# Kernel optimization log

Hardware: AMD Instinct MI355X
Metric: run time of the kernel (lower is better)

Reference implementation:

```python
import jax, jax.numpy as jnp
import numpy as np
import math

B, N = 1, 768
C_S, C_Z, C_H, H, P_QK, P_V = 256, 128, 128, 8, 8, 12
EPS, INF, LN_EPS = 1e-8, 1e5, 1e-5


def _quat_to_rot(q):
    # q: [..., 4] normalized quaternion (w, x, y, z) -> [..., 3, 3]
    w, x, y, z = jnp.moveaxis(q, -1, 0)
    r = jnp.stack([
        1 - 2 * (y * y + z * z), 2 * (x * y - w * z), 2 * (x * z + w * y),
        2 * (x * y + w * z), 1 - 2 * (x * x + z * z), 2 * (y * z - w * x),
        2 * (x * z - w * y), 2 * (y * z + w * x), 1 - 2 * (x * x + y * y),
    ], axis=-1)
    return r.reshape(q.shape[:-1] + (3, 3))


def _ln(x, g, b):
    mu = x.mean(-1, keepdims=True)
    var = ((x - mu) ** 2).mean(-1, keepdims=True)
    return (x - mu) * jax.lax.rsqrt(var + LN_EPS) * g + b


def setup_inputs():
    key = jax.random.key(0)
    ks = jax.random.split(key, 20)
    inp = {}
    inp['s'] = jax.random.normal(ks[0], (B, N, C_S), jnp.float32)
    inp['p'] = jax.random.normal(ks[1], (B, N, N, C_Z), jnp.float32)
    q = jax.random.normal(ks[2], (B, N, 4), jnp.float32)
    inp['rot'] = _quat_to_rot(q / jnp.linalg.norm(q, axis=-1, keepdims=True))
    inp['trans'] = 10.0 * jax.random.normal(ks[3], (B, N, 3), jnp.float32)
    inp['mask'] = jnp.ones((B, N), jnp.float32)
    concat_dim = H * C_H + H * P_V * 4 + H * C_Z
    dims = {'q': (H * C_H, C_S), 'kv': (2 * H * C_H, C_S), 'qp': (H * P_QK * 3, C_S),
            'kvp': (H * (P_QK + P_V) * 3, C_S), 'pb': (H, C_Z), 'o': (C_S, concat_dim),
            't1': (C_S, C_S), 't2': (C_S, C_S), 't3': (C_S, C_S), 'bb': (6, C_S)}
    i = 4
    for nm, (do, di) in dims.items():
        k1, k2 = jax.random.split(ks[i]); i += 1
        inp['W' + nm] = 0.02 * jax.random.normal(k1, (do, di), jnp.float32)
        inp['b' + nm] = 0.02 * jax.random.normal(k2, (do,), jnp.float32)
    inp['head_w'] = 0.1 * jax.random.normal(ks[i], (H,), jnp.float32)
    inp['g1'] = jnp.ones((C_S,), jnp.float32)
    inp['be1'] = jnp.zeros((C_S,), jnp.float32)
    inp['g2'] = jnp.ones((C_S,), jnp.float32)
    inp['be2'] = jnp.zeros((C_S,), jnp.float32)
    return inp


def reference(s, p, rot, trans, mask, Wq, bq, Wkv, bkv, Wqp, bqp, Wkvp, bkvp,
              Wpb, bpb, Wo, bo, Wt1, bt1, Wt2, bt2, Wt3, bt3, Wbb, bbb,
              head_w, g1, be1, g2, be2):
    # ---------------- Invariant Point Attention ----------------
    q = (s @ Wq.T + bq).reshape(B, N, H, C_H)
    kv = (s @ Wkv.T + bkv).reshape(B, N, H, 2 * C_H)
    k, v = kv[..., :C_H], kv[..., C_H:]
    # points: linear output is coordinate-major (x-block, y-block, z-block)
    qp = (s @ Wqp.T + bqp).reshape(B, N, 3, H, P_QK)
    qp = jnp.einsum('bnij,bnjhp->bnhpi', rot, qp) + trans[:, :, None, None, :]
    kvp = (s @ Wkvp.T + bkvp).reshape(B, N, 3, H, P_QK + P_V)
    kvp = jnp.einsum('bnij,bnjhp->bnhpi', rot, kvp) + trans[:, :, None, None, :]
    kp, vp = kvp[..., :P_QK, :], kvp[..., P_QK:, :]
    bias_p = p @ Wpb.T + bpb  # [B,N,N,H]
    a = jnp.einsum('bihc,bjhc->bhij', q, k) * math.sqrt(1.0 / (3 * C_H))
    a = a + math.sqrt(1.0 / 3) * jnp.transpose(bias_p, (0, 3, 1, 2))
    d2 = ((qp[:, :, None] - kp[:, None]) ** 2).sum(-1)  # [B,N,N,H,Pqk]
    hw = jax.nn.softplus(head_w) * math.sqrt(1.0 / (3 * (P_QK * 9.0 / 2)))
    pt_att = -0.5 * (d2 * hw[None, None, None, :, None]).sum(-1)  # [B,N,N,H]
    m2 = mask[:, :, None] * mask[:, None, :]
    a = a + jnp.transpose(pt_att, (0, 3, 1, 2)) + (INF * (m2 - 1.0))[:, None]
    att = jax.nn.softmax(a, axis=-1)  # [B,H,N,N]
    o = jnp.einsum('bhij,bjhc->bihc', att, v).reshape(B, N, H * C_H)
    opt = jnp.einsum('bhij,bjhpx->bihpx', att, vp)  # [B,N,H,Pv,3] global
    opt = jnp.einsum('bnji,bnhpj->bnhpi', rot, opt - trans[:, :, None, None, :])
    opt_norm = jnp.sqrt((opt ** 2).sum(-1) + EPS).reshape(B, N, H * P_V)
    opt_flat = jnp.moveaxis(opt.reshape(B, N, H * P_V, 3), -1, -2).reshape(B, N, 3 * H * P_V)
    opair = jnp.einsum('bhij,bijz->bihz', att, p).reshape(B, N, H * C_Z)
    ipa_out = jnp.concatenate([o, opt_flat, opt_norm, opair], -1) @ Wo.T + bo
    # residual + dropout(eval: identity) + LayerNorm
    s1 = _ln(s + ipa_out, g1, be1)
    # ---------------- StructureTransition (1 layer) ----------------
    x = jax.nn.relu(s1 @ Wt1.T + bt1)
    x = jax.nn.relu(x @ Wt2.T + bt2)
    s2 = _ln(s1 + (x @ Wt3.T + bt3), g2, be2)
    # ---------------- BackboneUpdate + masked quaternion compose ----------------
    upd = (s2 @ Wbb.T + bbb) * mask[..., None]  # [B,N,6]
    qvec = jnp.concatenate([jnp.ones(upd.shape[:-1] + (1,), upd.dtype), upd[..., :3]], -1)
    qvec = qvec / jnp.linalg.norm(qvec, axis=-1, keepdims=True)
    rot_new = jnp.einsum('bnij,bnjk->bnik', rot, _quat_to_rot(qvec))
    trans_new = trans + jnp.einsum('bnij,bnj->bni', rot, upd[..., 3:])
    return (s2, rot_new, trans_new)
```

## Files before the change

kernel.cpp:

```cpp
#include <hip/hip_runtime.h>
#include <hip/hip_bf16.h>
#include <math.h>

#define NN 768
#define CS 256
#define CZ 128
#define CH 128
#define HH 8
#define PQK 8
#define PV 12
#define CONCAT 2432
#define ATT_HSTRIDE (768*768)

typedef __bf16 v8bf __attribute__((ext_vector_type(8)));
typedef __bf16 v4bf __attribute__((ext_vector_type(4)));
typedef float  v4f  __attribute__((ext_vector_type(4)));

__device__ inline unsigned short f2bf(float f) {
    union { float f; unsigned u; } v; v.f = f;
    unsigned r = v.u + 0x7FFFu + ((v.u >> 16) & 1u);
    return (unsigned short)(r >> 16);
}
__device__ inline float bf2f(unsigned short u) {
    union { unsigned u; float f; } v; v.u = ((unsigned)u) << 16; return v.f;
}
__device__ inline unsigned encf(float f) {
    unsigned u = __float_as_uint(f);
    return (u >> 31) ? ~u : (u | 0x80000000u);
}
__device__ inline float decf(unsigned e) {
    unsigned u = (e >> 31) ? (e & 0x7FFFFFFFu) : ~e;
    return __uint_as_float(u);
}

#define NCVT 9
struct CvtDesc {
    const float* src[NCVT];
    unsigned short* dst[NCVT];
    int nelem[NCVT];
    int blk_start[NCVT + 1];
};

__global__ __launch_bounds__(256) void cvt_many(CvtDesc d)
{
    int b = blockIdx.x;
    int seg = 0;
    #pragma unroll
    for (int i = 0; i < NCVT - 1; i++) if (b >= d.blk_start[i + 1]) seg = i + 1;
    int local = b - d.blk_start[seg];
    int base = local * 2048 + threadIdx.x;
    const float* s = d.src[seg];
    unsigned short* o = d.dst[seg];
    int n = d.nelem[seg];
    #pragma unroll
    for (int r = 0; r < 8; r++) {
        int idx = base + r * 256;
        if (idx < n) o[idx] = f2bf(s[idx]);
    }
}

struct ProjDesc {
    const unsigned short* W[4];
    const float* bias[4];
    unsigned short* dstb[4];
    float* dstf[4];
    int D[4];
    int ldc[4];
    int mode[4];
    int blk_start[5];
};

__global__ __launch_bounds__(256) void proj_all(const unsigned short* __restrict__ A, ProjDesc d)
{
    __shared__ unsigned short As[64][40];
    __shared__ unsigned short Ws[64][40];
    int bx = blockIdx.x;
    int seg = 0;
    #pragma unroll
    for (int q = 0; q < 3; q++) if (bx >= d.blk_start[q + 1]) seg = q + 1;
    int bd = (bx - d.blk_start[seg]) * 64;
    int bi = blockIdx.y * 64;
    const unsigned short* W = d.W[seg];
    int D = d.D[seg], ldc = d.ldc[seg];

    int tid = threadIdx.x, lane = tid & 63, wid = tid >> 6;
    int wr = (wid >> 1) * 32, wc = (wid & 1) * 32;
    v4f acc[2][2] = {};
    int lrow = tid >> 2, lcol = (tid & 3) * 8;
    const unsigned short* Ap = A + (size_t)(bi + lrow) * 256 + lcol;
    const unsigned short* Wp = W + (size_t)(bd + lrow) * 256 + lcol;
    bool wv = (bd + lrow) < D;
    int fr = lane & 15, fc = (lane >> 4) * 8;

    for (int k0 = 0; k0 < 256; k0 += 32) {
        *(int4*)&As[lrow][lcol] = *(const int4*)(Ap + k0);
        int4 wz = {0, 0, 0, 0};
        *(int4*)&Ws[lrow][lcol] = wv ? *(const int4*)(Wp + k0) : wz;
        __syncthreads();
        v8bf a0 = *(const v8bf*)&As[wr + fr][fc];
        v8bf a1 = *(const v8bf*)&As[wr + 16 + fr][fc];
        v8bf b0 = *(const v8bf*)&Ws[wc + fr][fc];
        v8bf b1 = *(const v8bf*)&Ws[wc + 16 + fr][fc];
        acc[0][0] = __builtin_amdgcn_mfma_f32_16x16x32_bf16(a0, b0, acc[0][0], 0, 0, 0);
        acc[0][1] = __builtin_amdgcn_mfma_f32_16x16x32_bf16(a0, b1, acc[0][1], 0, 0, 0);
        acc[1][0] = __builtin_amdgcn_mfma_f32_16x16x32_bf16(a1, b0, acc[1][0], 0, 0, 0);
        acc[1][1] = __builtin_amdgcn_mfma_f32_16x16x32_bf16(a1, b1, acc[1][1], 0, 0, 0);
        __syncthreads();
    }
    const float* bias = d.bias[seg];
    int mode = d.mode[seg];
    unsigned short* Cb = d.dstb[seg];
    float* Cf = d.dstf[seg];
    int mrow = (lane >> 4) * 4;
    #pragma unroll
    for (int mi = 0; mi < 2; mi++) {
        #pragma unroll
        for (int ni = 0; ni < 2; ni++) {
            int dd = bd + wc + ni * 16 + fr;
            if (dd < D) {
                #pragma unroll
                for (int r = 0; r < 4; r++) {
                    int m = bi + wr + mi * 16 + mrow + r;
                    float v = acc[mi][ni][r] + bias[dd];
                    if (mode == 2) Cb[(size_t)m * ldc + dd] = f2bf(v);
                    else           Cf[(size_t)m * ldc + dd] = v;
                }
            }
        }
    }
}

template<int SPLITK, int MODE, int RELU>
__global__ __launch_bounds__(256) void mfma_gemm(
    const unsigned short* __restrict__ A,
    const unsigned short* __restrict__ W,
    const float* __restrict__ bias,
    float* __restrict__ C,
    unsigned short* __restrict__ Cb,
    int D, int K, int ldc)
{
    __shared__ unsigned short As[64][40];
    __shared__ unsigned short Ws[64][40];
    int tid = threadIdx.x;
    int bi = blockIdx.y * 64;
    int bd = blockIdx.x * 64;
    int kpb = K / SPLITK;
    int k0b = blockIdx.z * kpb;
    int lane = tid & 63;
    int wid = tid >> 6;
    int wr = (wid >> 1) * 32, wc = (wid & 1) * 32;
    v4f acc[2][2] = {};
    int lrow = tid >> 2;
    int lcol = (tid & 3) * 8;
    const unsigned short* Ap = A + (size_t)(bi + lrow) * K + lcol;
    const unsigned short* Wp = W + (size_t)(bd + lrow) * K + lcol;
    bool wv = (bd + lrow) < D;
    int fr = lane & 15, fc = (lane >> 4) * 8;

    for (int k0 = k0b; k0 < k0b + kpb; k0 += 32) {
        *(int4*)&As[lrow][lcol] = *(const int4*)(Ap + k0);
        int4 wz = {0, 0, 0, 0};
        *(int4*)&Ws[lrow][lcol] = wv ? *(const int4*)(Wp + k0) : wz;
        __syncthreads();
        v8bf a0 = *(const v8bf*)&As[wr + fr][fc];
        v8bf a1 = *(const v8bf*)&As[wr + 16 + fr][fc];
        v8bf b0 = *(const v8bf*)&Ws[wc + fr][fc];
        v8bf b1 = *(const v8bf*)&Ws[wc + 16 + fr][fc];
        acc[0][0] = __builtin_amdgcn_mfma_f32_16x16x32_bf16(a0, b0, acc[0][0], 0, 0, 0);
        acc[0][1] = __builtin_amdgcn_mfma_f32_16x16x32_bf16(a0, b1, acc[0][1], 0, 0, 0);
        acc[1][0] = __builtin_amdgcn_mfma_f32_16x16x32_bf16(a1, b0, acc[1][0], 0, 0, 0);
        acc[1][1] = __builtin_amdgcn_mfma_f32_16x16x32_bf16(a1, b1, acc[1][1], 0, 0, 0);
        __syncthreads();
    }
    int mrow = (lane >> 4) * 4;
    #pragma unroll
    for (int mi = 0; mi < 2; mi++) {
        #pragma unroll
        for (int ni = 0; ni < 2; ni++) {
            int d = bd + wc + ni * 16 + fr;
            if (d < D) {
                #pragma unroll
                for (int r = 0; r < 4; r++) {
                    int m = bi + wr + mi * 16 + mrow + r;
                    float v = acc[mi][ni][r];
                    if (SPLITK > 1) {
                        atomicAdd(&C[(size_t)m * ldc + d], v);
                    } else {
                        v += bias[d];
                        if (RELU) v = fmaxf(v, 0.f);
                        if (MODE != 2) C[(size_t)m * ldc + d] = v;
                        if (MODE >= 1) Cb[(size_t)m * ldc + d] = f2bf(v);
                    }
                }
            }
        }
    }
}

__global__ __launch_bounds__(256) void prep2_kernel(
    const float* __restrict__ qpraw, const float* __restrict__ kvpraw,
    const float* __restrict__ rot, const float* __restrict__ trans,
    const unsigned short* __restrict__ kv_bf,
    unsigned short* __restrict__ qph, unsigned short* __restrict__ qpl,
    unsigned short* __restrict__ kph, unsigned short* __restrict__ kpl,
    unsigned short* __restrict__ Vc)
{
    __shared__ unsigned short tile[32][136];
    int bx = blockIdx.x;
    int t = threadIdx.x;
    if (bx < 672) {
        int id = bx*256 + t;
        int i = id / (HH*28);
        int rem = id % (HH*28);
        int h = rem / 28;
        int idx = rem % 28;
        const float* R = rot + i*9;
        const float* T = trans + i*3;
        float s0, s1, s2;
        if (idx < 8) {
            s0 = qpraw[i*192 +   0 + h*8 + idx];
            s1 = qpraw[i*192 +  64 + h*8 + idx];
            s2 = qpraw[i*192 + 128 + h*8 + idx];
        } else {
            int pp = idx - 8;
            s0 = kvpraw[i*480 +   0 + h*20 + pp];
            s1 = kvpraw[i*480 + 160 + h*20 + pp];
            s2 = kvpraw[i*480 + 320 + h*20 + pp];
        }
        float ov[3];
        ov[0] = R[0]*s0 + R[1]*s1 + R[2]*s2 + T[0];
        ov[1] = R[3]*s0 + R[4]*s1 + R[5]*s2 + T[1];
        ov[2] = R[6]*s0 + R[7]*s1 + R[8]*s2 + T[2];
        if (idx < 8) {
            #pragma unroll
            for (int x = 0; x < 3; x++) {
                unsigned short hi = f2bf(ov[x]);
                qph[i*256 + h*32 + idx*3 + x] = hi;
                qpl[i*256 + h*32 + idx*3 + x] = f2bf(ov[x] - bf2f(hi));
            }
            if (idx == 0) {
                #pragma unroll
                for (int m = 24; m < 32; m++) { qph[i*256+h*32+m] = 0; qpl[i*256+h*32+m] = 0; }
            }
        } else if (idx < 16) {
            int pp = idx - 8;
            #pragma unroll
            for (int x = 0; x < 3; x++) {
                unsigned short hi = f2bf(ov[x]);
                kph[i*256 + h*32 + pp*3 + x] = hi;
                kpl[i*256 + h*32 + pp*3 + x] = f2bf(ov[x] - bf2f(hi));
            }
            if (idx == 8) {
                #pragma unroll
                for (int m = 24; m < 32; m++) { kph[i*256+h*32+m] = 0; kpl[i*256+h*32+m] = 0; }
            }
        } else {
            int ppv = idx - 16;
            #pragma unroll
            for (int x = 0; x < 3; x++)
                Vc[((size_t)h*192 + 128 + ppv*3 + x)*768 + i] = f2bf(ov[x]);
        }
    } else {
        int bx2 = bx - 672;
        int h = bx2 & 7, jt = bx2 >> 3;
        int r = t >> 3, c0 = (t & 7) * 16;
        const unsigned short* src = kv_bf + (size_t)(jt*32 + r)*2048 + h*256 + 128 + c0;
        *(int4*)&tile[r][c0]     = *(const int4*)src;
        *(int4*)&tile[r][c0 + 8] = *(const int4*)(src + 8);
        __syncthreads();
        int c = t >> 1, jh = (t & 1) * 16;
        unsigned short tmp[16];
        #pragma unroll
        for (int k = 0; k < 16; k++) tmp[k] = tile[jh + k][c];
        unsigned short* dst = Vc + ((size_t)h*192 + c)*768 + jt*32 + jh;
        *(int4*)dst       = *(int4*)&tmp[0];
        *(int4*)(dst + 8) = *(int4*)&tmp[8];
    }
}

__global__ __launch_bounds__(256) void logits_mfma(
    const unsigned short* __restrict__ q_bf, const unsigned short* __restrict__ kv_bf,
    const unsigned short* __restrict__ qph, const unsigned short* __restrict__ qpl,
    const unsigned short* __restrict__ kph, const unsigned short* __restrict__ kpl,
    const float* __restrict__ mask, const float* __restrict__ head_w,
    float* __restrict__ att, unsigned* __restrict__ m0enc)
{
    __shared__ unsigned short Qs[64][136];
    __shared__ unsigned short Ks[64][136];
    __shared__ unsigned short Aph[64][40], Apl[64][40], Bph[64][40], Bpl[64][40];
    __shared__ float Qss[64], Kss[64], Mi[64], Mj[64];
    int h = blockIdx.z;
    int i0 = blockIdx.y * 64, j0 = blockIdx.x * 64;
    int tid = threadIdx.x, lane = tid & 63, wid = tid >> 6;
    int wr = (wid >> 1) * 32, wc = (wid & 1) * 32;
    int r = tid >> 2, cq = (tid & 3) * 32;
    const unsigned short* qg = q_bf  + (size_t)(i0 + r)*1024 + h*128 + cq;
    const unsigned short* kg = kv_bf + (size_t)(j0 + r)*2048 + h*256 + cq;
    #pragma unroll
    for (int kk = 0; kk < 4; kk++) {
        *(int4*)&Qs[r][cq + kk*8] = *(const int4*)(qg + kk*8);
        *(int4*)&Ks[r][cq + kk*8] = *(const int4*)(kg + kk*8);
    }
    int cp = (tid & 3) * 8;
    *(int4*)&Aph[r][cp] = *(const int4*)(qph + (size_t)(i0 + r)*256 + h*32 + cp);
    *(int4*)&Apl[r][cp] = *(const int4*)(qpl + (size_t)(i0 + r)*256 + h*32 + cp);
    *(int4*)&Bph[r][cp] = *(const int4*)(kph + (size_t)(j0 + r)*256 + h*32 + cp);
    *(int4*)&Bpl[r][cp] = *(const int4*)(kpl + (size_t)(j0 + r)*256 + h*32 + cp);
    if (tid < 64) {
        Mi[tid] = mask[i0 + tid];
        Mj[tid] = mask[j0 + tid];
    }
    __syncthreads();
    if (tid < 64) {
        float qs2 = 0.f, ks2 = 0.f;
        #pragma unroll
        for (int m = 0; m < 24; m++) {
            float qv = bf2f(Aph[tid][m]) + bf2f(Apl[tid][m]);
            float kv = bf2f(Bph[tid][m]) + bf2f(Bpl[tid][m]);
            qs2 += qv*qv; ks2 += kv*kv;
        }
        Qss[tid] = qs2; Kss[tid] = ks2;
    }
    int fr = lane & 15, fc = (lane >> 4) * 8;
    v4f aqk[2][2] = {}, ap[2][2] = {};
    #pragma unroll
    for (int ks = 0; ks < 4; ks++) {
        v8bf a0 = *(const v8bf*)&Qs[wr + fr][ks*32 + fc];
        v8bf a1 = *(const v8bf*)&Qs[wr + 16 + fr][ks*32 + fc];
        v8bf b0 = *(const v8bf*)&Ks[wc + fr][ks*32 + fc];
        v8bf b1 = *(const v8bf*)&Ks[wc + 16 + fr][ks*32 + fc];
        aqk[0][0] = __builtin_amdgcn_mfma_f32_16x16x32_bf16(a0, b0, aqk[0][0], 0, 0, 0);
        aqk[0][1] = __builtin_amdgcn_mfma_f32_16x16x32_bf16(a0, b1, aqk[0][1], 0, 0, 0);
        aqk[1][0] = __builtin_amdgcn_mfma_f32_16x16x32_bf16(a1, b0, aqk[1][0], 0, 0, 0);
        aqk[1][1] = __builtin_amdgcn_mfma_f32_16x16x32_bf16(a1, b1, aqk[1][1], 0, 0, 0);
    }
    {
        v8bf ah0 = *(const v8bf*)&Aph[wr + fr][fc];
        v8bf ah1 = *(const v8bf*)&Aph[wr + 16 + fr][fc];
        v8bf al0 = *(const v8bf*)&Apl[wr + fr][fc];
        v8bf al1 = *(const v8bf*)&Apl[wr + 16 + fr][fc];
        v8bf bh0 = *(const v8bf*)&Bph[wc + fr][fc];
        v8bf bh1 = *(const v8bf*)&Bph[wc + 16 + fr][fc];
        v8bf bl0 = *(const v8bf*)&Bpl[wc + fr][fc];
        v8bf bl1 = *(const v8bf*)&Bpl[wc + 16 + fr][fc];
        ap[0][0] = __builtin_amdgcn_mfma_f32_16x16x32_bf16(ah0, bh0, ap[0][0], 0, 0, 0);
        ap[0][1] = __builtin_amdgcn_mfma_f32_16x16x32_bf16(ah0, bh1, ap[0][1], 0, 0, 0);
        ap[1][0] = __builtin_amdgcn_mfma_f32_16x16x32_bf16(ah1, bh0, ap[1][0], 0, 0, 0);
        ap[1][1] = __builtin_amdgcn_mfma_f32_16x16x32_bf16(ah1, bh1, ap[1][1], 0, 0, 0);
        ap[0][0] = __builtin_amdgcn_mfma_f32_16x16x32_bf16(ah0, bl0, ap[0][0], 0, 0, 0);
        ap[0][1] = __builtin_amdgcn_mfma_f32_16x16x32_bf16(ah0, bl1, ap[0][1], 0, 0, 0);
        ap[1][0] = __builtin_amdgcn_mfma_f32_16x16x32_bf16(ah1, bl0, ap[1][0], 0, 0, 0);
        ap[1][1] = __builtin_amdgcn_mfma_f32_16x16x32_bf16(ah1, bl1, ap[1][1], 0, 0, 0);
        ap[0][0] = __builtin_amdgcn_mfma_f32_16x16x32_bf16(al0, bh0, ap[0][0], 0, 0, 0);
        ap[0][1] = __builtin_amdgcn_mfma_f32_16x16x32_bf16(al0, bh1, ap[0][1], 0, 0, 0);
        ap[1][0] = __builtin_amdgcn_mfma_f32_16x16x32_bf16(al1, bh0, ap[1][0], 0, 0, 0);
        ap[1][1] = __builtin_amdgcn_mfma_f32_16x16x32_bf16(al1, bh1, ap[1][1], 0, 0, 0);
    }
    __syncthreads();
    float hx = head_w[h];
    float sp = (hx > 20.f) ? hx : log1pf(__expf(hx));
    float hw = sp * 0.09622504486493764f;
    const float scale_qk = 0.05103103630798288f;
    int mrow = (lane >> 4) * 4;
    float val[2][2][4];
    #pragma unroll
    for (int mi = 0; mi < 2; mi++) {
        #pragma unroll
        for (int ni = 0; ni < 2; ni++) {
            int jl = wc + ni*16 + fr;
            #pragma unroll
            for (int rr = 0; rr < 4; rr++) {
                int il = wr + mi*16 + mrow + rr;
                float v = aqk[mi][ni][rr]*scale_qk + hw*ap[mi][ni][rr]
                        - 0.5f*hw*(Qss[il] + Kss[jl])
                        + 100000.0f*(Mi[il]*Mj[jl] - 1.0f);
                val[mi][ni][rr] = v;
                att[(size_t)h*ATT_HSTRIDE + (size_t)(i0 + il)*768 + (j0 + jl)] = v;
            }
        }
    }
    #pragma unroll
    for (int mi = 0; mi < 2; mi++) {
        #pragma unroll
        for (int rr = 0; rr < 4; rr++) {
            float m = fmaxf(val[mi][0][rr], val[mi][1][rr]);
            #pragma unroll
            for (int d2 = 1; d2 < 16; d2 <<= 1) m = fmaxf(m, __shfl_xor(m, d2));
            if (fr == 0) {
                int il = wr + mi*16 + mrow + rr;
                atomicMax(&m0enc[h*768 + i0 + il], encf(m));
            }
        }
    }
}

__global__ __launch_bounds__(256) void fused_p3s_kernel(
    const float* __restrict__ att0,
    const float* __restrict__ p,
    const float* __restrict__ Wpb, const float* __restrict__ bpb,
    const unsigned* __restrict__ m0enc,
    unsigned short* __restrict__ att_bf,
    float* __restrict__ lpart,
    float* __restrict__ opart)
{
    __shared__ unsigned short ptile[64][132];
    __shared__ unsigned short wt[16][72];
    __shared__ float bpb_s[8], m8[8], lsum_w[4][8];

    int i = blockIdx.x;
    int half = blockIdx.y;
    int jbase = half * 384;
    int tid = threadIdx.x, lane = tid & 63, wid = tid >> 6;
    int fr = lane & 15, fc = (lane >> 4) * 8;
    int mrow = (lane >> 4) * 4;

    for (int idx = tid; idx < 16*72; idx += 256) ((unsigned short*)wt)[idx] = 0;
    if (tid < 8) {
        bpb_s[tid] = bpb[tid];
        m8[tid] = decf(m0enc[tid*768 + i]);
    }

    v8bf aW[4];
    #pragma unroll
    for (int ks = 0; ks < 4; ks++) {
        v8bf v = {};
        if (fr < 8) {
            const float* wp = Wpb + fr*128 + ks*32 + fc;
            float4 w0 = *(const float4*)wp;
            float4 w1 = *(const float4*)(wp + 4);
            v[0] = (__bf16)w0.x; v[1] = (__bf16)w0.y; v[2] = (__bf16)w0.z; v[3] = (__bf16)w0.w;
            v[4] = (__bf16)w1.x; v[5] = (__bf16)w1.y; v[6] = (__bf16)w1.z; v[7] = (__bf16)w1.w;
        }
        aW[ks] = v;
    }
    __syncthreads();
    float m0l[4];
    #pragma unroll
    for (int r = 0; r < 4; r++) m0l[r] = (mrow == 0) ? m8[r] : m8[4 + r];

    const float* pbase = p + (size_t)i*98304 + (size_t)jbase*128;
    float4 pfA[4], pfB[4];
    #pragma unroll
    for (int r = 0; r < 4; r++) {
        int idx = r*256 + tid;
        const float* src = pbase + (idx >> 4)*128 + (idx & 15)*8;
        pfA[r] = *(const float4*)src;
        pfB[r] = *(const float4*)(src + 4);
    }

    v4f accD[2] = {};
    float lacc[4] = {0.f, 0.f, 0.f, 0.f};
    const float sqrt13 = 0.57735026918962576f;
    bool expo = (mrow < 8);

    for (int t64 = 0; t64 < 6; t64++) {
        int j0 = jbase + t64 * 64;
        #pragma unroll
        for (int r = 0; r < 4; r++) {
            int idx = r*256 + tid;
            int j = idx >> 4, zo = (idx & 15) * 8;
            v4bf lo, hi;
            lo[0] = (__bf16)pfA[r].x; lo[1] = (__bf16)pfA[r].y;
            lo[2] = (__bf16)pfA[r].z; lo[3] = (__bf16)pfA[r].w;
            hi[0] = (__bf16)pfB[r].x; hi[1] = (__bf16)pfB[r].y;
            hi[2] = (__bf16)pfB[r].z; hi[3] = (__bf16)pfB[r].w;
            *(v4bf*)&ptile[j][zo]     = lo;
            *(v4bf*)&ptile[j][zo + 4] = hi;
        }
        if (t64 < 5) {
            #pragma unroll
            for (int r = 0; r < 4; r++) {
                int idx = r*256 + tid;
                const float* src = pbase + (size_t)((t64+1)*64 + (idx >> 4))*128 + (idx & 15)*8;
                pfA[r] = *(const float4*)src;
                pfB[r] = *(const float4*)(src + 4);
            }
        }
        __syncthreads();

        float a0v[4];
        if (expo) {
            int j = 16*wid + fr;
            #pragma unroll
            for (int r = 0; r < 4; r++)
                a0v[r] = att0[((size_t)(mrow + r)*768 + i)*768 + j0 + j];
        }

        v4f bd = {};
        #pragma unroll
        for (int ks = 0; ks < 4; ks++) {
            int c = ks*32 + fc;
            v4bf blo = *(const v4bf*)&ptile[16*wid + fr][c];
            v4bf bhi = *(const v4bf*)&ptile[16*wid + fr][c + 4];
            v8bf b;
            b[0]=blo[0]; b[1]=blo[1]; b[2]=blo[2]; b[3]=blo[3];
            b[4]=bhi[0]; b[5]=bhi[1]; b[6]=bhi[2]; b[7]=bhi[3];
            bd = __builtin_amdgcn_mfma_f32_16x16x32_bf16(aW[ks], b, bd, 0, 0, 0);
        }

        if (expo) {
            int j = 16*wid + fr;
            float w8[4];
            #pragma unroll
            for (int r = 0; r < 4; r++) {
                int h = mrow + r;
                float L = a0v[r] + sqrt13*(bd[r] + bpb_s[h]);
                w8[r] = __expf(fminf(L - m0l[r], 60.f));
            }
            #pragma unroll
            for (int r = 0; r < 4; r++) {
                int h = mrow + r;
                unsigned short wb = f2bf(w8[r]);
                wt[h][j] = wb;
                att_bf[((size_t)h*768 + i)*768 + j0 + j] = wb;
            }
            #pragma unroll
            for (int m = 1; m < 16; m <<= 1) {
                #pragma unroll
                for (int r = 0; r < 4; r++) w8[r] += __shfl_xor(w8[r], m);
            }
            #pragma unroll
            for (int r = 0; r < 4; r++) lacc[r] += w8[r];
        }
        __syncthreads();

        #pragma unroll
        for (int mm = 0; mm < 2; mm++) {
            int zcol = (2*wid + mm)*16 + fr;
            #pragma unroll
            for (int ks = 0; ks < 2; ks++) {
                v8bf b;
                #pragma unroll
                for (int kk = 0; kk < 8; kk++)
                    b[kk] = *(const __bf16*)&ptile[ks*32 + fc + kk][zcol];
                v8bf a = *(const v8bf*)&wt[fr][ks*32 + fc];
                accD[mm] = __builtin_amdgcn_mfma_f32_16x16x32_bf16(a, b, accD[mm], 0, 0, 0);
            }
        }
        __syncthreads();
    }

    if (fr == 0 && expo) {
        #pragma unroll
        for (int r = 0; r < 4; r++) lsum_w[wid][mrow + r] = lacc[r];
    }
    __syncthreads();
    if (tid < 8) {
        lpart[(size_t)(half*8 + tid)*768 + i] =
            lsum_w[0][tid] + lsum_w[1][tid] + lsum_w[2][tid] + lsum_w[3][tid];
    }
    if (expo) {
        float* ob = opart + (size_t)(half*768 + i)*1024;
        #pragma unroll
        for (int mm = 0; mm < 2; mm++) {
            int z = (2*wid + mm)*16 + fr;
            #pragma unroll
            for (int r = 0; r < 4; r++)
                ob[(mrow + r)*128 + z] = accD[mm][r];
        }
    }
}

__global__ __launch_bounds__(256) void preduce_kernel(
    const float* __restrict__ lpart, const float* __restrict__ opart,
    float* __restrict__ linv, unsigned short* __restrict__ concat)
{
    __shared__ float inv_s[8];
    int i = blockIdx.x, t = threadIdx.x;
    if (t < 8) {
        float l = lpart[(size_t)t*768 + i] + lpart[(size_t)(8 + t)*768 + i];
        float iv = 1.0f / l;
        inv_s[t] = iv;
        linv[(size_t)t*768 + i] = iv;
    }
    __syncthreads();
    const float* o0 = opart + (size_t)i*1024;
    const float* o1 = opart + (size_t)(768 + i)*1024;
    #pragma unroll
    for (int k = 0; k < 4; k++) {
        int c = t + k*256;
        float s = o0[c] + o1[c];
        concat[(size_t)i*CONCAT + 1408 + c] = f2bf(s * inv_s[c >> 7]);
    }
}

__global__ __launch_bounds__(256) void attvc_mfma(
    const unsigned short* __restrict__ att_bf, const unsigned short* __restrict__ Vc,
    const float* __restrict__ linv, const float* __restrict__ rot,
    const float* __restrict__ trans, unsigned short* __restrict__ concat)
{
    __shared__ unsigned short As[64][72];
    __shared__ unsigned short Bs[64][72];
    int h = blockIdx.z;
    int i0 = blockIdx.y * 64, nd0 = blockIdx.x * 64;
    int tid = threadIdx.x, lane = tid & 63, wid = tid >> 6;
    int wr = (wid >> 1) * 32, wc = (wid & 1) * 32;
    int r = tid >> 2, c8 = (tid & 3) * 16;
    int fr = lane & 15, fc = (lane >> 4) * 8;
    v4f acc[2][2] = {};
    for (int k0 = 0; k0 < 768; k0 += 64) {
        const unsigned short* ag = att_bf + ((size_t)h*768 + i0 + r)*768 + k0 + c8;
        const unsigned short* bg = Vc + ((size_t)h*192 + nd0 + r)*768 + k0 + c8;
        *(int4*)&As[r][c8]     = *(const int4*)ag;
        *(int4*)&As[r][c8 + 8] = *(const int4*)(ag + 8);
        *(int4*)&Bs[r][c8]     = *(const int4*)bg;
        *(int4*)&Bs[r][c8 + 8] = *(const int4*)(bg + 8);
        __syncthreads();
        #pragma unroll
        for (int ks = 0; ks < 2; ks++) {
            v8bf a0 = *(const v8bf*)&As[wr + fr][ks*32 + fc];
            v8bf a1 = *(const v8bf*)&As[wr + 16 + fr][ks*32 + fc];
            v8bf b0 = *(const v8bf*)&Bs[wc + fr][ks*32 + fc];
            v8bf b1 = *(const v8bf*)&Bs[wc + 16 + fr][ks*32 + fc];
            acc[0][0] = __builtin_amdgcn_mfma_f32_16x16x32_bf16(a0, b0, acc[0][0], 0, 0, 0);
            acc[0][1] = __builtin_amdgcn_mfma_f32_16x16x32_bf16(a0, b1, acc[0][1], 0, 0, 0);
            acc[1][0] = __builtin_amdgcn_mfma_f32_16x16x32_bf16(a1, b0, acc[1][0], 0, 0, 0);
            acc[1][1] = __builtin_amdgcn_mfma_f32_16x16x32_bf16(a1, b1, acc[1][1], 0, 0, 0);
        }
        __syncthreads();
    }
    int mrow = (lane >> 4) * 4;
    float lv[2][4];
    #pragma unroll
    for (int mi = 0; mi < 2; mi++) {
        int ibase = i0 + wr + mi*16 + mrow;
        float4 l4 = *(const float4*)&linv[(size_t)h*768 + ibase];
        lv[mi][0] = l4.x; lv[mi][1] = l4.y; lv[mi][2] = l4.z; lv[mi][3] = l4.w;
    }
    if (nd0 < 128) {
        #pragma unroll
        for (int mi = 0; mi < 2; mi++) {
            #pragma unroll
            for (int ni = 0; ni < 2; ni++) {
                int d = nd0 + wc + ni*16 + fr;
                #pragma unroll
                for (int rr = 0; rr < 4; rr++) {
                    int i = i0 + wr + mi*16 + mrow + rr;
                    concat[(size_t)i*CONCAT + h*128 + d] = f2bf(acc[mi][ni][rr] * lv[mi][rr]);
                }
            }
        }
    } else {
        float* opt_s = (float*)&As[0][0];
        #pragma unroll
        for (int mi = 0; mi < 2; mi++) {
            #pragma unroll
            for (int ni = 0; ni < 2; ni++) {
                int c = wc + ni*16 + fr;
                if (c < 36) {
                    #pragma unroll
                    for (int rr = 0; rr < 4; rr++) {
                        int rl = wr + mi*16 + mrow + rr;
                        opt_s[rl*36 + c] = acc[mi][ni][rr] * lv[mi][rr];
                    }
                }
            }
        }
        __syncthreads();
        for (int it = tid; it < 768; it += 256) {
            int rl = it / 12, pp = it % 12;
            int i = i0 + rl;
            const float* R = rot + i*9;
            const float* T = trans + i*3;
            float y0 = opt_s[rl*36 + pp*3 + 0] - T[0];
            float y1 = opt_s[rl*36 + pp*3 + 1] - T[1];
            float y2 = opt_s[rl*36 + pp*3 + 2] - T[2];
            float o0 = R[0]*y0 + R[3]*y1 + R[6]*y2;
            float o1 = R[1]*y0 + R[4]*y1 + R[7]*y2;
            float o2 = R[2]*y0 + R[5]*y1 + R[8]*y2;
            float nrm = sqrtf(o0*o0 + o1*o1 + o2*o2 + 1e-8f);
            int hp = h*12 + pp;
            unsigned short* cb = concat + (size_t)i*CONCAT;
            cb[1024 +   0 + hp] = f2bf(o0);
            cb[1024 +  96 + hp] = f2bf(o1);
            cb[1024 + 192 + hp] = f2bf(o2);
            cb[1312 + hp] = f2bf(nrm);
        }
    }
}

__global__ __launch_bounds__(256) void tail_kernel(
    const float* __restrict__ s, const float* __restrict__ ipa,
    const float* __restrict__ bo,
    const float* __restrict__ g1, const float* __restrict__ be1,
    const unsigned short* __restrict__ Wt1, const float* __restrict__ bt1,
    const unsigned short* __restrict__ Wt2, const float* __restrict__ bt2,
    const unsigned short* __restrict__ Wt3, const float* __restrict__ bt3,
    const float* __restrict__ g2, const float* __restrict__ be2,
    const float* __restrict__ Wbb, const float* __restrict__ bbb,
    const float* __restrict__ mask,
    const float* __restrict__ rot, const float* __restrict__ trans,
    float* __restrict__ out, float* __restrict__ rot_out, float* __restrict__ trans_out)
{
    __shared__ float s1f[32][257];
    __shared__ unsigned short Ab[32][264];
    __shared__ float upd_s[32][6];
    int i0 = blockIdx.x * 32;
    int tid = threadIdx.x, lane = tid & 63, wid = tid >> 6;
    int fr = lane & 15, fc = (lane >> 4) * 8, mrow = (lane >> 4) * 4;

    int r = tid >> 3, cg = (tid & 7) * 32;
    {
        float xv[32];
        float sum = 0.f, sq = 0.f;
        #pragma unroll
        for (int q = 0; q < 8; q++) {
            float4 a = *(const float4*)&s[(size_t)(i0 + r)*256 + cg + q*4];
            float4 b = *(const float4*)&ipa[(size_t)(i0 + r)*256 + cg + q*4];
            float4 c = *(const float4*)&bo[cg + q*4];
            float v0 = a.x + b.x + c.x, v1 = a.y + b.y + c.y;
            float v2 = a.z + b.z + c.z, v3 = a.w + b.w + c.w;
            xv[q*4+0] = v0; xv[q*4+1] = v1; xv[q*4+2] = v2; xv[q*4+3] = v3;
            sum += v0 + v1 + v2 + v3;
            sq  += v0*v0 + v1*v1 + v2*v2 + v3*v3;
        }
        #pragma unroll
        for (int d = 1; d < 8; d <<= 1) { sum += __shfl_xor(sum, d); sq += __shfl_xor(sq, d); }
        float mu = sum * (1.0f/256.0f);
        float var = sq * (1.0f/256.0f) - mu*mu;
        float rsig = 1.0f / sqrtf(var + 1e-5f);
        #pragma unroll
        for (int c = 0; c < 32; c++) {
            float o = (xv[c] - mu) * rsig * g1[cg + c] + be1[cg + c];
            s1f[r][cg + c] = o;
            Ab[r][cg + c] = f2bf(o);
        }
    }
    __syncthreads();

    const unsigned short* Ws[3] = {Wt1, Wt2, Wt3};
    const float* Bs[3] = {bt1, bt2, bt3};
    #pragma unroll
    for (int stage = 0; stage < 3; stage++) {
        const unsigned short* W = Ws[stage];
        const float* bias = Bs[stage];
        v4f acc[2][4] = {};
        #pragma unroll
        for (int k0 = 0; k0 < 8; k0++) {
            v8bf a0 = *(const v8bf*)&Ab[fr][k0*32 + fc];
            v8bf a1 = *(const v8bf*)&Ab[16 + fr][k0*32 + fc];
            #pragma unroll
            for (int n = 0; n < 4; n++) {
                int d = wid*64 + n*16 + fr;
                v8bf b = *(const v8bf*)&W[(size_t)d*256 + k0*32 + fc];
                acc[0][n] = __builtin_amdgcn_mfma_f32_16x16x32_bf16(a0, b, acc[0][n], 0, 0, 0);
                acc[1][n] = __builtin_amdgcn_mfma_f32_16x16x32_bf16(a1, b, acc[1][n], 0, 0, 0);
            }
        }
        __syncthreads();
        if (stage < 2) {
            #pragma unroll
            for (int mi = 0; mi < 2; mi++) {
                #pragma unroll
                for (int n = 0; n < 4; n++) {
                    int d = wid*64 + n*16 + fr;
                    #pragma unroll
                    for (int rr = 0; rr < 4; rr++) {
                        int m = mi*16 + mrow + rr;
                        Ab[m][d] = f2bf(fmaxf(acc[mi][n][rr] + bias[d], 0.f));
                    }
                }
            }
        } else {
            #pragma unroll
            for (int mi = 0; mi < 2; mi++) {
                #pragma unroll
                for (int n = 0; n < 4; n++) {
                    int d = wid*64 + n*16 + fr;
                    #pragma unroll
                    for (int rr = 0; rr < 4; rr++) {
                        int m = mi*16 + mrow + rr;
                        s1f[m][d] += acc[mi][n][rr] + bias[d];
                    }
                }
            }
        }
        __syncthreads();
    }

    {
        float xv[32];
        float sum = 0.f, sq = 0.f;
        #pragma unroll
        for (int c = 0; c < 32; c++) {
            float v = s1f[r][cg + c];
            xv[c] = v; sum += v; sq += v*v;
        }
        #pragma unroll
        for (int d = 1; d < 8; d <<= 1) { sum += __shfl_xor(sum, d); sq += __shfl_xor(sq, d); }
        float mu = sum * (1.0f/256.0f);
        float var = sq * (1.0f/256.0f) - mu*mu;
        float rsig = 1.0f / sqrtf(var + 1e-5f);
        float o4[32];
        #pragma unroll
        for (int c = 0; c < 32; c++)
            o4[c] = (xv[c] - mu) * rsig * g2[cg + c] + be2[cg + c];
        #pragma unroll
        for (int q = 0; q < 8; q++) {
            float4 w; w.x = o4[q*4]; w.y = o4[q*4+1]; w.z = o4[q*4+2]; w.w = o4[q*4+3];
            *(float4*)&out[(size_t)(i0 + r)*256 + cg + q*4] = w;
        }
        __syncthreads();
        #pragma unroll
        for (int c = 0; c < 32; c++) s1f[r][cg + c] = o4[c];
    }
    __syncthreads();

    if (tid < 192) {
        int rr = tid / 6, d = tid % 6;
        float acc = bbb[d];
        const float* wb = Wbb + d*256;
        #pragma unroll 8
        for (int c = 0; c < 256; c++) acc += s1f[rr][c] * wb[c];
        upd_s[rr][d] = acc * mask[i0 + rr];
    }
    __syncthreads();

    if (tid < 32) {
        int i = i0 + tid;
        float u0 = upd_s[tid][0], u1 = upd_s[tid][1], u2 = upd_s[tid][2];
        float t0 = upd_s[tid][3], t1 = upd_s[tid][4], t2 = upd_s[tid][5];
        float n = sqrtf(1.f + u0*u0 + u1*u1 + u2*u2);
        float w = 1.f/n, x = u0/n, y = u1/n, z = u2/n;
        float R[3][3];
        R[0][0] = 1.f - 2.f*(y*y + z*z); R[0][1] = 2.f*(x*y - w*z);       R[0][2] = 2.f*(x*z + w*y);
        R[1][0] = 2.f*(x*y + w*z);       R[1][1] = 1.f - 2.f*(x*x + z*z); R[1][2] = 2.f*(y*z - w*x);
        R[2][0] = 2.f*(x*z - w*y);       R[2][1] = 2.f*(y*z + w*x);       R[2][2] = 1.f - 2.f*(x*x + y*y);
        const float* Ri = rot + i*9;
        #pragma unroll
        for (int a = 0; a < 3; a++) {
            #pragma unroll
            for (int b = 0; b < 3; b++) {
                float acc = 0.f;
                #pragma unroll
                for (int j = 0; j < 3; j++) acc += Ri[a*3+j]*R[j][b];
                rot_out[i*9 + a*3 + b] = acc;
            }
            trans_out[i*3 + a] = trans[i*3 + a] + Ri[a*3+0]*t0 + Ri[a*3+1]*t1 + Ri[a*3+2]*t2;
        }
    }
}

extern "C" void kernel_launch(void* const* d_in, const int* in_sizes, int n_in,
                              void* d_out, int out_size, void* d_ws, size_t ws_size,
                              hipStream_t stream)
{
    const float* s      = (const float*)d_in[0];
    const float* p      = (const float*)d_in[1];
    const float* rot    = (const float*)d_in[2];
    const float* trans  = (const float*)d_in[3];
    const float* mask   = (const float*)d_in[4];
    const float* Wq     = (const float*)d_in[5];
    const float* bq     = (const float*)d_in[6];
    const float* Wkv    = (const float*)d_in[7];
    const float* bkv    = (const float*)d_in[8];
    const float* Wqp    = (const float*)d_in[9];
    const float* bqp    = (const float*)d_in[10];
    const float* Wkvp   = (const float*)d_in[11];
    const float* bkvp   = (const float*)d_in[12];
    const float* Wpb    = (const float*)d_in[13];
    const float* bpb    = (const float*)d_in[14];
// ... 96 lines not shown
```

Before: 192.7 us.

## Double-buffer pair tile in fused p3s kernel; load point operands directly to registers in logits

In the logits kernel, the point-query and point-key fragments are now loaded straight from global memory into MFMA registers, and the squared norms are computed with wave shuffles. This removes the shared-memory staging and one barrier. In the fused pair kernel, the p tile becomes double-buffered in LDS, so the next tile's bf16 conversion and store, plus the global prefetch two tiles ahead, overlap with the current tile's compute. This removes one barrier per iteration, at the cost of doubling the ptile shared memory and raising register pressure.

```diff
diff --git a/kernel.cpp b/kernel.cpp
--- a/kernel.cpp
+++ b/kernel.cpp
@@ -287,8 +287,7 @@
 {
     __shared__ unsigned short Qs[64][136];
     __shared__ unsigned short Ks[64][136];
-    __shared__ unsigned short Aph[64][40], Apl[64][40], Bph[64][40], Bpl[64][40];
-    __shared__ float Qss[64], Kss[64], Mi[64], Mj[64];
+    __shared__ float Mi[64], Mj[64];
     int h = blockIdx.z;
     int i0 = blockIdx.y * 64, j0 = blockIdx.x * 64;
     int tid = threadIdx.x, lane = tid & 63, wid = tid >> 6;
@@ -301,28 +300,49 @@
         *(int4*)&Qs[r][cq + kk*8] = *(const int4*)(qg + kk*8);
         *(int4*)&Ks[r][cq + kk*8] = *(const int4*)(kg + kk*8);
     }
-    int cp = (tid & 3) * 8;
-    *(int4*)&Aph[r][cp] = *(const int4*)(qph + (size_t)(i0 + r)*256 + h*32 + cp);
-    *(int4*)&Apl[r][cp] = *(const int4*)(qpl + (size_t)(i0 + r)*256 + h*32 + cp);
-    *(int4*)&Bph[r][cp] = *(const int4*)(kph + (size_t)(j0 + r)*256 + h*32 + cp);
-    *(int4*)&Bpl[r][cp] = *(const int4*)(kpl + (size_t)(j0 + r)*256 + h*32 + cp);
     if (tid < 64) {
         Mi[tid] = mask[i0 + tid];
         Mj[tid] = mask[j0 + tid];
     }
+    int fr = lane & 15, fc = (lane >> 4) * 8;
+    v8bf ah0 = *(const v8bf*)&qph[(size_t)(i0 + wr + fr)*256 + h*32 + fc];
+    v8bf ah1 = *(const v8bf*)&qph[(size_t)(i0 + wr + 16 + fr)*256 + h*32 + fc];
+    v8bf al0 = *(const v8bf*)&qpl[(size_t)(i0 + wr + fr)*256 + h*32 + fc];
+    v8bf al1 = *(const v8bf*)&qpl[(size_t)(i0 + wr + 16 + fr)*256 + h*32 + fc];
+    v8bf bh0 = *(const v8bf*)&kph[(size_t)(j0 + wc + fr)*256 + h*32 + fc];
+    v8bf bh1 = *(const v8bf*)&kph[(size_t)(j0 + wc + 16 + fr)*256 + h*32 + fc];
+    v8bf bl0 = *(const v8bf*)&kpl[(size_t)(j0 + wc + fr)*256 + h*32 + fc];
+    v8bf bl1 = *(const v8bf*)&kpl[(size_t)(j0 + wc + 16 + fr)*256 + h*32 + fc];
+    float q2a = 0.f, q2b = 0.f, k2a = 0.f, k2b = 0.f;
+    #pragma unroll
+    for (int m = 0; m < 8; m++) {
+        float va = (float)ah0[m] + (float)al0[m];
+        float vb = (float)ah1[m] + (float)al1[m];
+        float wa = (float)bh0[m] + (float)bl0[m];
+        float wb = (float)bh1[m] + (float)bl1[m];
+        q2a += va*va; q2b += vb*vb; k2a += wa*wa; k2b += wb*wb;
+    }
+    q2a += __shfl_xor(q2a, 16); q2a += __shfl_xor(q2a, 32);
+    q2b += __shfl_xor(q2b, 16); q2b += __shfl_xor(q2b, 32);
+    k2a += __shfl_xor(k2a, 16); k2a += __shfl_xor(k2a, 32);
+    k2b += __shfl_xor(k2b, 16); k2b += __shfl_xor(k2b, 32);
+
+    v4f ap[2][2] = {};
+    ap[0][0] = __builtin_amdgcn_mfma_f32_16x16x32_bf16(ah0, bh0, ap[0][0], 0, 0, 0);
+    ap[0][1] = __builtin_amdgcn_mfma_f32_16x16x32_bf16(ah0, bh1, ap[0][1], 0, 0, 0);
+    ap[1][0] = __builtin_amdgcn_mfma_f32_16x16x32_bf16(ah1, bh0, ap[1][0], 0, 0, 0);
+    ap[1][1] = __builtin_amdgcn_mfma_f32_16x16x32_bf16(ah1, bh1, ap[1][1], 0, 0, 0);
+    ap[0][0] = __builtin_amdgcn_mfma_f32_16x16x32_bf16(ah0, bl0, ap[0][0], 0, 0, 0);
+    ap[0][1] = __builtin_amdgcn_mfma_f32_16x16x32_bf16(ah0, bl1, ap[0][1], 0, 0, 0);
+    ap[1][0] = __builtin_amdgcn_mfma_f32_16x16x32_bf16(ah1, bl0, ap[1][0], 0, 0, 0);
+    ap[1][1] = __builtin_amdgcn_mfma_f32_16x16x32_bf16(ah1, bl1, ap[1][1], 0, 0, 0);
+    ap[0][0] = __builtin_amdgcn_mfma_f32_16x16x32_bf16(al0, bh0, ap[0][0], 0, 0, 0);
+    ap[0][1] = __builtin_amdgcn_mfma_f32_16x16x32_bf16(al0, bh1, ap[0][1], 0, 0, 0);
+    ap[1][0] = __builtin_amdgcn_mfma_f32_16x16x32_bf16(al1, bh0, ap[1][0], 0, 0, 0);
+    ap[1][1] = __builtin_amdgcn_mfma_f32_16x16x32_bf16(al1, bh1, ap[1][1], 0, 0, 0);
+
     __syncthreads();
-    if (tid < 64) {
-        float qs2 = 0.f, ks2 = 0.f;
-        #pragma unroll
-        for (int m = 0; m < 24; m++) {
-            float qv = bf2f(Aph[tid][m]) + bf2f(Apl[tid][m]);
-            float kv = bf2f(Bph[tid][m]) + bf2f(Bpl[tid][m]);
-            qs2 += qv*qv; ks2 += kv*kv;
-        }
-        Qss[tid] = qs2; Kss[tid] = ks2;
-    }
-    int fr = lane & 15, fc = (lane >> 4) * 8;
-    v4f aqk[2][2] = {}, ap[2][2] = {};
+    v4f aqk[2][2] = {};
     #pragma unroll
     for (int ks = 0; ks < 4; ks++) {
         v8bf a0 = *(const v8bf*)&Qs[wr + fr][ks*32 + fc];
@@ -334,29 +354,6 @@
         aqk[1][0] = __builtin_amdgcn_mfma_f32_16x16x32_bf16(a1, b0, aqk[1][0], 0, 0, 0);
         aqk[1][1] = __builtin_amdgcn_mfma_f32_16x16x32_bf16(a1, b1, aqk[1][1], 0, 0, 0);
     }
-    {
-        v8bf ah0 = *(const v8bf*)&Aph[wr + fr][fc];
-        v8bf ah1 = *(const v8bf*)&Aph[wr + 16 + fr][fc];
-        v8bf al0 = *(const v8bf*)&Apl[wr + fr][fc];
-        v8bf al1 = *(const v8bf*)&Apl[wr + 16 + fr][fc];
-        v8bf bh0 = *(const v8bf*)&Bph[wc + fr][fc];
-        v8bf bh1 = *(const v8bf*)&Bph[wc + 16 + fr][fc];
-        v8bf bl0 = *(const v8bf*)&Bpl[wc + fr][fc];
-        v8bf bl1 = *(const v8bf*)&Bpl[wc + 16 + fr][fc];
-        ap[0][0] = __builtin_amdgcn_mfma_f32_16x16x32_bf16(ah0, bh0, ap[0][0], 0, 0, 0);
-        ap[0][1] = __builtin_amdgcn_mfma_f32_16x16x32_bf16(ah0, bh1, ap[0][1], 0, 0, 0);
-        ap[1][0] = __builtin_amdgcn_mfma_f32_16x16x32_bf16(ah1, bh0, ap[1][0], 0, 0, 0);
-        ap[1][1] = __builtin_amdgcn_mfma_f32_16x16x32_bf16(ah1, bh1, ap[1][1], 0, 0, 0);
-        ap[0][0] = __builtin_amdgcn_mfma_f32_16x16x32_bf16(ah0, bl0, ap[0][0], 0, 0, 0);
-        ap[0][1] = __builtin_amdgcn_mfma_f32_16x16x32_bf16(ah0, bl1, ap[0][1], 0, 0, 0);
-        ap[1][0] = __builtin_amdgcn_mfma_f32_16x16x32_bf16(ah1, bl0, ap[1][0], 0, 0, 0);
-        ap[1][1] = __builtin_amdgcn_mfma_f32_16x16x32_bf16(ah1, bl1, ap[1][1], 0, 0, 0);
-        ap[0][0] = __builtin_amdgcn_mfma_f32_16x16x32_bf16(al0, bh0, ap[0][0], 0, 0, 0);
-        ap[0][1] = __builtin_amdgcn_mfma_f32_16x16x32_bf16(al0, bh1, ap[0][1], 0, 0, 0);
-        ap[1][0] = __builtin_amdgcn_mfma_f32_16x16x32_bf16(al1, bh0, ap[1][0], 0, 0, 0);
-        ap[1][1] = __builtin_amdgcn_mfma_f32_16x16x32_bf16(al1, bh1, ap[1][1], 0, 0, 0);
-    }
-    __syncthreads();
     float hx = head_w[h];
     float sp = (hx > 20.f) ? hx : log1pf(__expf(hx));
     float hw = sp * 0.09622504486493764f;
@@ -366,13 +363,15 @@
     #pragma unroll
     for (int mi = 0; mi < 2; mi++) {
         #pragma unroll
-        for (int ni = 0; ni < 2; ni++) {
-            int jl = wc + ni*16 + fr;
-            #pragma unroll
-            for (int rr = 0; rr < 4; rr++) {
+        for (int rr = 0; rr < 4; rr++) {
+            float qss = __shfl((mi == 0) ? q2a : q2b, mrow + rr);
+            #pragma unroll
+            for (int ni = 0; ni < 2; ni++) {
+                int jl = wc + ni*16 + fr;
                 int il = wr + mi*16 + mrow + rr;
+                float kss = (ni == 0) ? k2a : k2b;
                 float v = aqk[mi][ni][rr]*scale_qk + hw*ap[mi][ni][rr]
-                        - 0.5f*hw*(Qss[il] + Kss[jl])
+                        - 0.5f*hw*(qss + kss)
                         + 100000.0f*(Mi[il]*Mj[jl] - 1.0f);
                 val[mi][ni][rr] = v;
                 att[(size_t)h*ATT_HSTRIDE + (size_t)(i0 + il)*768 + (j0 + jl)] = v;
@@ -403,7 +402,7 @@
     float* __restrict__ lpart,
     float* __restrict__ opart)
 {
-    __shared__ unsigned short ptile[64][132];
+    __shared__ unsigned short ptile[2][64][132];
     __shared__ unsigned short wt[16][72];
     __shared__ float bpb_s[8], m8[8], lsum_w[4][8];
 
@@ -433,20 +432,36 @@
         }
         aW[ks] = v;
     }
+
+    const float* pbase = p + (size_t)i*98304 + (size_t)jbase*128;
+    int ldrow = tid >> 4, ldz = (tid & 15) * 8;
+    float4 pfA[4], pfB[4];
+    #pragma unroll
+    for (int r2 = 0; r2 < 4; r2++) {
+        const float* src = pbase + (size_t)(r2*16 + ldrow)*128 + ldz;
+        pfA[r2] = *(const float4*)src;
+        pfB[r2] = *(const float4*)(src + 4);
+    }
+    #pragma unroll
+    for (int r2 = 0; r2 < 4; r2++) {
+        v4bf lo, hi;
+        lo[0] = (__bf16)pfA[r2].x; lo[1] = (__bf16)pfA[r2].y;
+        lo[2] = (__bf16)pfA[r2].z; lo[3] = (__bf16)pfA[r2].w;
+        hi[0] = (__bf16)pfB[r2].x; hi[1] = (__bf16)pfB[r2].y;
+        hi[2] = (__bf16)pfB[r2].z; hi[3] = (__bf16)pfB[r2].w;
+        *(v4bf*)&ptile[0][r2*16 + ldrow][ldz]     = lo;
+        *(v4bf*)&ptile[0][r2*16 + ldrow][ldz + 4] = hi;
+    }
+    #pragma unroll
+    for (int r2 = 0; r2 < 4; r2++) {
+        const float* src = pbase + (size_t)(64 + r2*16 + ldrow)*128 + ldz;
+        pfA[r2] = *(const float4*)src;
+        pfB[r2] = *(const float4*)(src + 4);
+    }
     __syncthreads();
     float m0l[4];
     #pragma unroll
-    for (int r = 0; r < 4; r++) m0l[r] = (mrow == 0) ? m8[r] : m8[4 + r];
-
-    const float* pbase = p + (size_t)i*98304 + (size_t)jbase*128;
-    float4 pfA[4], pfB[4];
-    #pragma unroll
-    for (int r = 0; r < 4; r++) {
-        int idx = r*256 + tid;
-        const float* src = pbase + (idx >> 4)*128 + (idx & 15)*8;
-        pfA[r] = *(const float4*)src;
-        pfB[r] = *(const float4*)(src + 4);
-    }
+    for (int r2 = 0; r2 < 4; r2++) m0l[r2] = (mrow == 0) ? m8[r2] : m8[4 + r2];
 
     v4f accD[2] = {};
     float lacc[4] = {0.f, 0.f, 0.f, 0.f};
@@ -454,73 +469,66 @@
     bool expo = (mrow < 8);
 
     for (int t64 = 0; t64 < 6; t64++) {
+        int cur = t64 & 1;
         int j0 = jbase + t64 * 64;
-        #pragma unroll
-        for (int r = 0; r < 4; r++) {
-            int idx = r*256 + tid;
-            int j = idx >> 4, zo = (idx & 15) * 8;
-            v4bf lo, hi;
-            lo[0] = (__bf16)pfA[r].x; lo[1] = (__bf16)pfA[r].y;
-            lo[2] = (__bf16)pfA[r].z; lo[3] = (__bf16)pfA[r].w;
-            hi[0] = (__bf16)pfB[r].x; hi[1] = (__bf16)pfB[r].y;
-            hi[2] = (__bf16)pfB[r].z; hi[3] = (__bf16)pfB[r].w;
-            *(v4bf*)&ptile[j][zo]     = lo;
-            *(v4bf*)&ptile[j][zo + 4] = hi;
-        }
-        if (t64 < 5) {
-            #pragma unroll
-            for (int r = 0; r < 4; r++) {
-                int idx = r*256 + tid;
-                const float* src = pbase + (size_t)((t64+1)*64 + (idx >> 4))*128 + (idx & 15)*8;
-                pfA[r] = *(const float4*)src;
-                pfB[r] = *(const float4*)(src + 4);
-            }
-        }
-        __syncthreads();
-
-        float a0v[4];
-        if (expo) {
-            int j = 16*wid + fr;
-            #pragma unroll
-            for (int r = 0; r < 4; r++)
-                a0v[r] = att0[((size_t)(mrow + r)*768 + i)*768 + j0 + j];
-        }
 
         v4f bd = {};
         #pragma unroll
         for (int ks = 0; ks < 4; ks++) {
             int c = ks*32 + fc;
-            v4bf blo = *(const v4bf*)&ptile[16*wid + fr][c];
-            v4bf bhi = *(const v4bf*)&ptile[16*wid + fr][c + 4];
+            v4bf blo = *(const v4bf*)&ptile[cur][16*wid + fr][c];
+            v4bf bhi = *(const v4bf*)&ptile[cur][16*wid + fr][c + 4];
             v8bf b;
             b[0]=blo[0]; b[1]=blo[1]; b[2]=blo[2]; b[3]=blo[3];
             b[4]=bhi[0]; b[5]=bhi[1]; b[6]=bhi[2]; b[7]=bhi[3];
             bd = __builtin_amdgcn_mfma_f32_16x16x32_bf16(aW[ks], b, bd, 0, 0, 0);
         }
-
         if (expo) {
             int j = 16*wid + fr;
-            float w8[4];
-            #pragma unroll
-            for (int r = 0; r < 4; r++) {
-                int h = mrow + r;
-                float L = a0v[r] + sqrt13*(bd[r] + bpb_s[h]);
-                w8[r] = __expf(fminf(L - m0l[r], 60.f));
-            }
-            #pragma unroll
-            for (int r = 0; r < 4; r++) {
-                int h = mrow + r;
-                unsigned short wb = f2bf(w8[r]);
+            float a0v[4], w8[4];
+            #pragma unroll
+            for (int r2 = 0; r2 < 4; r2++)
+                a0v[r2] = att0[((size_t)(mrow + r2)*768 + i)*768 + j0 + j];
+            #pragma unroll
+            for (int r2 = 0; r2 < 4; r2++) {
+                int h = mrow + r2;
+                float L = a0v[r2] + sqrt13*(bd[r2] + bpb_s[h]);
+                w8[r2] = __expf(fminf(L - m0l[r2], 60.f));
+            }
+            #pragma unroll
+            for (int r2 = 0; r2 < 4; r2++) {
+                int h = mrow + r2;
+                unsigned short wb = f2bf(w8[r2]);
                 wt[h][j] = wb;
                 att_bf[((size_t)h*768 + i)*768 + j0 + j] = wb;
             }
             #pragma unroll
             for (int m = 1; m < 16; m <<= 1) {
                 #pragma unroll
-                for (int r = 0; r < 4; r++) w8[r] += __shfl_xor(w8[r], m);
-            }
-            #pragma unroll
-            for (int r = 0; r < 4; r++) lacc[r] += w8[r];
+                for (int r2 = 0; r2 < 4; r2++) w8[r2] += __shfl_xor(w8[r2], m);
+            }
+            #pragma unroll
+            for (int r2 = 0; r2 < 4; r2++) lacc[r2] += w8[r2];
+        }
+        if (t64 < 5) {
+            #pragma unroll
+            for (int r2 = 0; r2 < 4; r2++) {
+                v4bf lo, hi;
+                lo[0] = (__bf16)pfA[r2].x; lo[1] = (__bf16)pfA[r2].y;
+                lo[2] = (__bf16)pfA[r2].z; lo[3] = (__bf16)pfA[r2].w;
+                hi[0] = (__bf16)pfB[r2].x; hi[1] = (__bf16)pfB[r2].y;
+                hi[2] = (__bf16)pfB[r2].z; hi[3] = (__bf16)pfB[r2].w;
+                *(v4bf*)&ptile[cur ^ 1][r2*16 + ldrow][ldz]     = lo;
+                *(v4bf*)&ptile[cur ^ 1][r2*16 + ldrow][ldz + 4] = hi;
+            }
+            if (t64 < 4) {
+                #pragma unroll
+                for (int r2 = 0; r2 < 4; r2++) {
+                    const float* src = pbase + (size_t)((t64+2)*64 + r2*16 + ldrow)*128 + ldz;
+                    pfA[r2] = *(const float4*)src;
+                    pfB[r2] = *(const float4*)(src + 4);
+                }
+            }
         }
         __syncthreads();
 
@@ -532,7 +540,7 @@
                 v8bf b;
                 #pragma unroll
                 for (int kk = 0; kk < 8; kk++)
-                    b[kk] = *(const __bf16*)&ptile[ks*32 + fc + kk][zcol];
+                    b[kk] = *(const __bf16*)&ptile[cur][ks*32 + fc + kk][zcol];
                 v8bf a = *(const v8bf*)&wt[fr][ks*32 + fc];
                 accD[mm] = __builtin_amdgcn_mfma_f32_16x16x32_bf16(a, b, accD[mm], 0, 0, 0);
             }
@@ -542,7 +550,7 @@
 
     if (fr == 0 && expo) {
         #pragma unroll
-        for (int r = 0; r < 4; r++) lsum_w[wid][mrow + r] = lacc[r];
+        for (int r2 = 0; r2 < 4; r2++) lsum_w[wid][mrow + r2] = lacc[r2];
     }
     __syncthreads();
     if (tid < 8) {
@@ -555,8 +563,8 @@
         for (int mm = 0; mm < 2; mm++) {
             int z = (2*wid + mm)*16 + fr;
             #pragma unroll
-            for (int r = 0; r < 4; r++)
-                ob[(mrow + r)*128 + z] = accD[mm][r];
+            for (int r2 = 0; r2 < 4; r2++)
+                ob[(mrow + r2)*128 + z] = accD[mm][r2];
         }
     }
 }
```

Result: faster. 187.0 us (median of 2 runs) (-3.0%).
